# Optimization experiments

Hardware: AMD Instinct MI355X
Metric: run time of the kernel (lower is better)

## Reference

```python
import jax, jax.numpy as jnp
import numpy as np


def _branch(x2d, V, U, v2, v1, u2, u1):
    # x2d: [N, in]; V: [s, in]; U: [out, s]; scales are [1, dim]
    Vq = jnp.sign(V)
    Uq = jnp.sign(U)
    v1u2 = v1 * u2  # [1, s]
    h = (x2d * v2) @ Vq.T          # [N, s]
    y = (h * v1u2) @ Uq.T          # [N, out]
    return y * u1


def setup_inputs() -> dict:
    key = jax.random.key(0)
    ks = jax.random.split(key, 14)
    IN, OUT, S = 4096, 4096, 1024
    B, T = 4, 2048
    f = jax.random.normal
    return {
        "x":    f(ks[0], (B, T, IN), jnp.float32),
        "V":    f(ks[1], (S, IN), jnp.float32),
        "U":    f(ks[2], (OUT, S), jnp.float32),
        "v2":   f(ks[3], (1, IN), jnp.float32),
        "v1":   f(ks[4], (1, S), jnp.float32),
        "u2":   f(ks[5], (1, S), jnp.float32),
        "u1":   f(ks[6], (1, OUT), jnp.float32),
        "V_R":  f(ks[7], (S, IN), jnp.float32),
        "U_R":  f(ks[8], (OUT, S), jnp.float32),
        "v2_R": f(ks[9], (1, IN), jnp.float32),
        "v1_R": f(ks[10], (1, S), jnp.float32),
        "u2_R": f(ks[11], (1, S), jnp.float32),
        "u1_R": f(ks[12], (1, OUT), jnp.float32),
        "bias": f(ks[13], (OUT,), jnp.float32),
    }


def reference(x, V, U, v2, v1, u2, u1, V_R, U_R, v2_R, v1_R, u2_R, u1_R, bias):
    *lead, hidden = x.shape
    x2d = x.reshape(-1, hidden)
    y = _branch(x2d, V, U, v2, v1, u2, u1)
    y = y + _branch(x2d, V_R, U_R, v2_R, v1_R, u2_R, u1_R)
    y = y + bias
    return y.reshape(*lead, bias.shape[0])
```

## Files before the change

### kernel.cpp

```cpp
#include <hip/hip_runtime.h>
#include <hip/hip_bf16.h>
#include <stdint.h>

typedef __bf16 bf16_t;
typedef __attribute__((ext_vector_type(8))) __bf16 bf16x8;
typedef __attribute__((ext_vector_type(4))) float f32x4;

#define DIM_IN  4096
#define DIM_OUT 4096
#define DIM_S   1024
#define DIM_S2  2048
#define NROWS   8192

typedef const __attribute__((address_space(1))) void gvoid_t;
typedef __attribute__((address_space(3))) void lvoid_t;

__device__ __forceinline__ float signf(float v) {
    return (v > 0.f) ? 1.f : ((v < 0.f) ? -1.f : 0.f);
}


__global__ void cast_x_kernel(const float* __restrict__ x, bf16_t* __restrict__ xb) {
    int idx = blockIdx.x * blockDim.x + threadIdx.x;
    const float4* p = reinterpret_cast<const float4*>(x) + (size_t)idx * 2;
    float4 a = p[0], b = p[1];
    bf16x8 o;
    o[0] = (bf16_t)a.x; o[1] = (bf16_t)a.y; o[2] = (bf16_t)a.z; o[3] = (bf16_t)a.w;
    o[4] = (bf16_t)b.x; o[5] = (bf16_t)b.y; o[6] = (bf16_t)b.z; o[7] = (bf16_t)b.w;
    reinterpret_cast<bf16x8*>(xb)[idx] = o;
}

__global__ void build_vcat_kernel(const float* __restrict__ V, const float* __restrict__ v2,
                                  const float* __restrict__ V_R, const float* __restrict__ v2_R,
                                  bf16_t* __restrict__ out) {
    int idx = blockIdx.x * blockDim.x + threadIdx.x;
    int s2 = idx >> 9;
    int i0 = (idx & 511) * 8;
    const float* src; const float* sc;
    if (s2 < DIM_S) { src = V   + (size_t)s2 * DIM_IN;           sc = v2;   }
    else            { src = V_R + (size_t)(s2 - DIM_S) * DIM_IN; sc = v2_R; }
    float4 a  = *reinterpret_cast<const float4*>(src + i0);
    float4 b  = *reinterpret_cast<const float4*>(src + i0 + 4);
    float4 sa = *reinterpret_cast<const float4*>(sc + i0);
    float4 sb = *reinterpret_cast<const float4*>(sc + i0 + 4);
    bf16x8 o;
    o[0] = (bf16_t)(signf(a.x) * sa.x); o[1] = (bf16_t)(signf(a.y) * sa.y);
    o[2] = (bf16_t)(signf(a.z) * sa.z); o[3] = (bf16_t)(signf(a.w) * sa.w);
    o[4] = (bf16_t)(signf(b.x) * sb.x); o[5] = (bf16_t)(signf(b.y) * sb.y);
    o[6] = (bf16_t)(signf(b.z) * sb.z); o[7] = (bf16_t)(signf(b.w) * sb.w);
    reinterpret_cast<bf16x8*>(out)[idx] = o;
}

__global__ void build_wcat_kernel(const float* __restrict__ U, const float* __restrict__ v1,
                                  const float* __restrict__ u2, const float* __restrict__ u1,
                                  const float* __restrict__ U_R, const float* __restrict__ v1_R,
                                  const float* __restrict__ u2_R, const float* __restrict__ u1_R,
                                  bf16_t* __restrict__ out) {
    int idx = blockIdx.x * blockDim.x + threadIdx.x;
    int j  = idx >> 8;
    int s0 = (idx & 255) * 8;
    const float* srcU; const float* sv1; const float* su2; float amp;
    if (s0 < DIM_S) { srcU = U   + (size_t)j * DIM_S + s0; sv1 = v1 + s0;   su2 = u2 + s0;   amp = u1[j];   }
    else { int s = s0 - DIM_S;
           srcU = U_R + (size_t)j * DIM_S + s;  sv1 = v1_R + s; su2 = u2_R + s; amp = u1_R[j]; }
    float4 a  = *reinterpret_cast<const float4*>(srcU);
    float4 b  = *reinterpret_cast<const float4*>(srcU + 4);
    float4 va = *reinterpret_cast<const float4*>(sv1);
    float4 vb = *reinterpret_cast<const float4*>(sv1 + 4);
    float4 ua = *reinterpret_cast<const float4*>(su2);
    float4 ub = *reinterpret_cast<const float4*>(su2 + 4);
    bf16x8 o;
    o[0] = (bf16_t)(amp * va.x * ua.x * signf(a.x));
    o[1] = (bf16_t)(amp * va.y * ua.y * signf(a.y));
    o[2] = (bf16_t)(amp * va.z * ua.z * signf(a.z));
    o[3] = (bf16_t)(amp * va.w * ua.w * signf(a.w));
    o[4] = (bf16_t)(amp * vb.x * ub.x * signf(b.x));
    o[5] = (bf16_t)(amp * vb.y * ub.y * signf(b.y));
    o[6] = (bf16_t)(amp * vb.z * ub.z * signf(b.z));
    o[7] = (bf16_t)(amp * vb.w * ub.w * signf(b.w));
    reinterpret_cast<bf16x8*>(out)[idx] = o;
}


#define VMCNT0() do { asm volatile("s_waitcnt vmcnt(0)" ::: "memory"); \
                      __builtin_amdgcn_sched_barrier(0); } while (0)

template<int N, int K, bool OUT_BF16>
__global__ __launch_bounds__(512, 2) void gemm256_kernel(
        const bf16_t* __restrict__ A, const bf16_t* __restrict__ B,
        bf16_t* __restrict__ Cb, float* __restrict__ Cf,
        const float* __restrict__ bias) {
    extern __shared__ char lds[];
    constexpr int NT = K / 64;
    static_assert(NT >= 2, "K too small");
    const int tid  = threadIdx.x;
    const int wave = tid >> 6;
    const int lane = tid & 63;
    const int wr = wave >> 2;
    const int wc = wave & 3;

    const int nwg  = gridDim.x;
    const int orig = blockIdx.x;
    const int swz  = (orig & 7) * (nwg >> 3) + (orig >> 3);
    constexpr int NTX = N / 256;
    const int n0 = (swz % NTX) * 256;
    const int m0 = (swz / NTX) * 256;

    char* ldsA = lds;
    char* ldsB = lds + 65536;

    const char* gA[2]; const char* gB[2];
#pragma unroll
    for (int j = 0; j < 2; ++j) {
        int off = j * 8192 + wave * 1024 + lane * 16;
        int lg  = off ^ (((off >> 7) & 7) << 4);
        int row = lg >> 7;
        int cb  = lg & 127;
        gA[j] = (const char*)A + (size_t)(m0 + row) * (K * 2) + cb;
        gB[j] = (const char*)B + (size_t)(n0 + row) * (K * 2) + cb;
    }

#define STAGE_A(t_, mh) do { \
    int _lo = (((t_) & 1) << 15) + ((mh) << 14) + (wave << 10); \
    size_t _ga = (size_t)(mh) * (128 * K * 2) + (size_t)(t_) * 128; \
    __builtin_amdgcn_global_load_lds((gvoid_t*)(gA[0] + _ga), (lvoid_t*)(ldsA + _lo), 16, 0, 0); \
    __builtin_amdgcn_global_load_lds((gvoid_t*)(gA[1] + _ga), (lvoid_t*)(ldsA + _lo + 8192), 16, 0, 0); \
} while (0)
#define STAGE_B(t_, nh) do { \
    int _lo = (((t_) & 1) << 15) + ((nh) << 14) + (wave << 10); \
    size_t _ga = (size_t)(nh) * (128 * K * 2) + (size_t)(t_) * 128; \
    __builtin_amdgcn_global_load_lds((gvoid_t*)(gB[0] + _ga), (lvoid_t*)(ldsB + _lo), 16, 0, 0); \
    __builtin_amdgcn_global_load_lds((gvoid_t*)(gB[1] + _ga), (lvoid_t*)(ldsB + _lo + 8192), 16, 0, 0); \
} while (0)

    const int swzmask = (lane & 7) << 4;
    int abase0, abase1, bbase0, bbase1;
    {
        int araw = (lane & 15) * 128 + ((lane >> 4) << 4);
        abase0 = (araw ^ swzmask) + (wr << 14);
        abase1 = ((araw + 64) ^ swzmask) + (wr << 14);
        int braw = ((wc & 1) * 64 + (lane & 15)) * 128 + ((lane >> 4) << 4);
        bbase0 = (braw ^ swzmask) + ((wc >> 1) << 14);
        bbase1 = ((braw + 64) ^ swzmask) + ((wc >> 1) << 14);
    }

#define RD_A4(dst, base, mg, t_) do { \
    const int _sb = (((t_) & 1) << 15) + (base); \
    _Pragma("unroll") \
    for (int mi = 0; mi < 4; ++mi) \
        dst[mi] = *(const bf16x8*)(ldsA + _sb + ((mg) * 4 + mi) * 2048); \
} while (0)
#define RD_B4(dst, base, t_) do { \
    const int _sb = (((t_) & 1) << 15) + (base); \
    _Pragma("unroll") \
    for (int ni = 0; ni < 4; ++ni) \
        dst[ni] = *(const bf16x8*)(ldsB + _sb + ni * 2048); \
} while (0)
#define MFMA16(mg, AF, BF) do { \
    __builtin_amdgcn_s_setprio(1); \
    _Pragma("unroll") \
    for (int mi = 0; mi < 4; ++mi) \
        _Pragma("unroll") \
        for (int n = 0; n < 4; ++n) \
            acc[(mg) * 4 + mi][n] = __builtin_amdgcn_mfma_f32_16x16x32_bf16( \
                AF[mi], BF[n], acc[(mg) * 4 + mi][n], 0, 0, 0); \
    __builtin_amdgcn_s_setprio(0); \
} while (0)

    f32x4 acc[8][4];
#pragma unroll
    for (int m = 0; m < 8; ++m)
#pragma unroll
        for (int n = 0; n < 4; ++n)
            acc[m][n] = (f32x4){0.f, 0.f, 0.f, 0.f};

    bf16x8 afA[4], afB[4], bf0[4], bf1[4];

    STAGE_A(0, 0); STAGE_A(0, 1);
    STAGE_B(0, 0); STAGE_B(0, 1);
    VMCNT0();
    __builtin_amdgcn_s_barrier();

    for (int t = 0; t < NT; ++t) {
        const bool i1 = (t + 1 < NT);
        RD_A4(afA, abase0, 0, t);
        RD_B4(bf0, bbase0, t);
        if (i1) { STAGE_A(t + 1, 0); STAGE_A(t + 1, 1); }
        MFMA16(0, afA, bf0);
        RD_A4(afB, abase0, 1, t);
        if (i1) { STAGE_B(t + 1, 0); STAGE_B(t + 1, 1); }
        MFMA16(1, afB, bf0);
        RD_A4(afA, abase1, 0, t);
        RD_B4(bf1, bbase1, t);
        MFMA16(0, afA, bf1);
        RD_A4(afB, abase1, 1, t);
        MFMA16(1, afB, bf1);
        if (i1) { VMCNT0(); }
        __builtin_amdgcn_s_barrier();
    }

#undef RD_A4
#undef RD_B4
#undef MFMA16
#undef STAGE_A
#undef STAGE_B

    const int cr = (lane >> 4) << 2;
    const int cc = lane & 15;
#pragma unroll
    for (int m = 0; m < 8; ++m) {
        const int row = m0 + wr * 128 + m * 16 + cr;
#pragma unroll
        for (int n = 0; n < 4; ++n) {
            const int col = n0 + wc * 64 + n * 16 + cc;
            if (OUT_BF16) {
#pragma unroll
                for (int j = 0; j < 4; ++j)
                    Cb[(size_t)(row + j) * N + col] = (bf16_t)acc[m][n][j];
            } else {
                const float bv = bias[col];
#pragma unroll
                for (int j = 0; j < 4; ++j)
                    Cf[(size_t)(row + j) * N + col] = acc[m][n][j] + bv;
            }
        }
    }
}

extern "C" void kernel_launch(void* const* d_in, const int* in_sizes, int n_in,
                              void* d_out, int out_size, void* d_ws, size_t ws_size,
                              hipStream_t stream) {
    const float* x    = (const float*)d_in[0];
    const float* V    = (const float*)d_in[1];
    const float* U    = (const float*)d_in[2];
    const float* v2   = (const float*)d_in[3];
    const float* v1   = (const float*)d_in[4];
    const float* u2   = (const float*)d_in[5];
    const float* u1   = (const float*)d_in[6];
    const float* V_R  = (const float*)d_in[7];
    const float* U_R  = (const float*)d_in[8];
    const float* v2_R = (const float*)d_in[9];
    const float* v1_R = (const float*)d_in[10];
    const float* u2_R = (const float*)d_in[11];
    const float* u1_R = (const float*)d_in[12];
    const float* bias = (const float*)d_in[13];
    float* out = (float*)d_out;

    char* ws = (char*)d_ws;
    bf16_t* Xb   = (bf16_t*)(ws);
    bf16_t* Vcat = (bf16_t*)(ws + (size_t)64  * 1024 * 1024);
    bf16_t* Wcat = (bf16_t*)(ws + (size_t)80  * 1024 * 1024);
    bf16_t* Hb   = (bf16_t*)(ws + (size_t)96  * 1024 * 1024);

    (void)hipFuncSetAttribute((const void*)gemm256_kernel<DIM_S2, DIM_IN, true>,
                              hipFuncAttributeMaxDynamicSharedMemorySize, 131072);
    (void)hipFuncSetAttribute((const void*)gemm256_kernel<DIM_OUT, DIM_S2, false>,
                              hipFuncAttributeMaxDynamicSharedMemorySize, 131072);

    cast_x_kernel    <<<16384, 256, 0, stream>>>(x, Xb);
    build_vcat_kernel<<<4096, 256, 0, stream>>>(V, v2, V_R, v2_R, Vcat);
    build_wcat_kernel<<<4096, 256, 0, stream>>>(U, v1, u2, u1, U_R, v1_R, u2_R, u1_R, Wcat);

    gemm256_kernel<DIM_S2, DIM_IN, true>
        <<<(DIM_S2 / 256) * (NROWS / 256), 512, 131072, stream>>>(Xb, Vcat, Hb, nullptr, nullptr);
    gemm256_kernel<DIM_OUT, DIM_S2, false>
        <<<(DIM_OUT / 256) * (NROWS / 256), 512, 131072, stream>>>(Hb, Wcat, nullptr, out, bias);
}
```

Baseline: 289.8 us.

## Switch GEMM inner loop to 32x32x16 MFMA with software-pipelined LDS reads

Replaces the 16x16x32 bf16 MFMA tiles with 32x32x16 MFMA tiles, restructuring LDS fragment offsets, swizzle and accumulator layout to match. The K-loop is software-pipelined with double-buffered register fragments so LDS reads for the next k-slice overlap the current MFMAs, including prefetching across the barrier into the next stage. Larger MFMA tiles cut LDS read traffic per flop and instruction count. The risk is a wrong swizzle or layout mapping and a less coalesced epilogue store pattern.

```diff
diff --git a/kernel.cpp b/kernel.cpp
--- a/kernel.cpp
+++ b/kernel.cpp
@@ -5,6 +5,7 @@
 typedef __bf16 bf16_t;
 typedef __attribute__((ext_vector_type(8))) __bf16 bf16x8;
 typedef __attribute__((ext_vector_type(4))) float f32x4;
+typedef __attribute__((ext_vector_type(16))) float f32x16;
 
 #define DIM_IN  4096
 #define DIM_OUT 4096
@@ -133,95 +134,96 @@
     __builtin_amdgcn_global_load_lds((gvoid_t*)(gB[1] + _ga), (lvoid_t*)(ldsB + _lo + 8192), 16, 0, 0); \
 } while (0)
 
-    const int swzmask = (lane & 7) << 4;
-    int abase0, abase1, bbase0, bbase1;
-    {
-        int araw = (lane & 15) * 128 + ((lane >> 4) << 4);
-        abase0 = (araw ^ swzmask) + (wr << 14);
-        abase1 = ((araw + 64) ^ swzmask) + (wr << 14);
-        int braw = ((wc & 1) * 64 + (lane & 15)) * 128 + ((lane >> 4) << 4);
-        bbase0 = (braw ^ swzmask) + ((wc >> 1) << 14);
-        bbase1 = ((braw + 64) ^ swzmask) + ((wc >> 1) << 14);
-    }
-
-#define RD_A4(dst, base, mg, t_) do { \
-    const int _sb = (((t_) & 1) << 15) + (base); \
+    const int hi = lane >> 5;
+    const int lk = lane & 7;
+    int oA[4], oB[4];
+#pragma unroll
+    for (int kk = 0; kk < 4; ++kk) {
+        int slot = (((kk << 1) | hi) ^ lk) << 4;
+        oA[kk] = (wr << 14) + (lane & 31) * 128 + slot;
+        oB[kk] = 65536 + ((wc >> 1) << 14) + ((wc & 1) << 13) + (lane & 31) * 128 + slot;
+    }
+
+#define RD_A(dst, kk) do { \
     _Pragma("unroll") \
     for (int mi = 0; mi < 4; ++mi) \
-        dst[mi] = *(const bf16x8*)(ldsA + _sb + ((mg) * 4 + mi) * 2048); \
-} while (0)
-#define RD_B4(dst, base, t_) do { \
-    const int _sb = (((t_) & 1) << 15) + (base); \
-    _Pragma("unroll") \
-    for (int ni = 0; ni < 4; ++ni) \
-        dst[ni] = *(const bf16x8*)(ldsB + _sb + ni * 2048); \
-} while (0)
-#define MFMA16(mg, AF, BF) do { \
+        dst[mi] = *(const bf16x8*)(lds + oA[kk] + mi * 4096); \
+} while (0)
+#define RD_B(dst, kk) do { \
+    _Pragma("unroll") \
+    for (int ni = 0; ni < 2; ++ni) \
+        dst[ni] = *(const bf16x8*)(lds + oB[kk] + ni * 4096); \
+} while (0)
+#define FLIP() do { \
+    _Pragma("unroll") \
+    for (int kk = 0; kk < 4; ++kk) { oA[kk] ^= 0x8000; oB[kk] ^= 0x8000; } \
+} while (0)
+#define MFMA8(AF, BF) do { \
     __builtin_amdgcn_s_setprio(1); \
     _Pragma("unroll") \
     for (int mi = 0; mi < 4; ++mi) \
         _Pragma("unroll") \
-        for (int n = 0; n < 4; ++n) \
-            acc[(mg) * 4 + mi][n] = __builtin_amdgcn_mfma_f32_16x16x32_bf16( \
-                AF[mi], BF[n], acc[(mg) * 4 + mi][n], 0, 0, 0); \
+        for (int ni = 0; ni < 2; ++ni) \
+            acc[mi][ni] = __builtin_amdgcn_mfma_f32_32x32x16_bf16( \
+                AF[mi], BF[ni], acc[mi][ni], 0, 0, 0); \
     __builtin_amdgcn_s_setprio(0); \
 } while (0)
 
-    f32x4 acc[8][4];
-#pragma unroll
-    for (int m = 0; m < 8; ++m)
-#pragma unroll
-        for (int n = 0; n < 4; ++n)
-            acc[m][n] = (f32x4){0.f, 0.f, 0.f, 0.f};
-
-    bf16x8 afA[4], afB[4], bf0[4], bf1[4];
+    f32x16 acc[4][2];
+#pragma unroll
+    for (int m = 0; m < 4; ++m)
+#pragma unroll
+        for (int n = 0; n < 2; ++n)
+#pragma unroll
+            for (int j = 0; j < 16; ++j)
+                acc[m][n][j] = 0.f;
+
+    bf16x8 afP[4], afQ[4], bfP[2], bfQ[2];
 
     STAGE_A(0, 0); STAGE_A(0, 1);
     STAGE_B(0, 0); STAGE_B(0, 1);
     VMCNT0();
     __builtin_amdgcn_s_barrier();
+    RD_A(afP, 0); RD_B(bfP, 0);
 
     for (int t = 0; t < NT; ++t) {
         const bool i1 = (t + 1 < NT);
-        RD_A4(afA, abase0, 0, t);
-        RD_B4(bf0, bbase0, t);
         if (i1) { STAGE_A(t + 1, 0); STAGE_A(t + 1, 1); }
-        MFMA16(0, afA, bf0);
-        RD_A4(afB, abase0, 1, t);
+        RD_A(afQ, 1); RD_B(bfQ, 1);
+        MFMA8(afP, bfP);
         if (i1) { STAGE_B(t + 1, 0); STAGE_B(t + 1, 1); }
-        MFMA16(1, afB, bf0);
-        RD_A4(afA, abase1, 0, t);
-        RD_B4(bf1, bbase1, t);
-        MFMA16(0, afA, bf1);
-        RD_A4(afB, abase1, 1, t);
-        MFMA16(1, afB, bf1);
+        RD_A(afP, 2); RD_B(bfP, 2);
+        MFMA8(afQ, bfQ);
+        RD_A(afQ, 3); RD_B(bfQ, 3);
+        MFMA8(afP, bfP);
         if (i1) { VMCNT0(); }
         __builtin_amdgcn_s_barrier();
-    }
-
-#undef RD_A4
-#undef RD_B4
-#undef MFMA16
+        if (i1) { FLIP(); RD_A(afP, 0); RD_B(bfP, 0); }
+        MFMA8(afQ, bfQ);
+    }
+
+#undef RD_A
+#undef RD_B
+#undef FLIP
+#undef MFMA8
 #undef STAGE_A
 #undef STAGE_B
 
-    const int cr = (lane >> 4) << 2;
-    const int cc = lane & 15;
-#pragma unroll
-    for (int m = 0; m < 8; ++m) {
-        const int row = m0 + wr * 128 + m * 16 + cr;
-#pragma unroll
-        for (int n = 0; n < 4; ++n) {
-            const int col = n0 + wc * 64 + n * 16 + cc;
-            if (OUT_BF16) {
-#pragma unroll
-                for (int j = 0; j < 4; ++j)
-                    Cb[(size_t)(row + j) * N + col] = (bf16_t)acc[m][n][j];
-            } else {
-                const float bv = bias[col];
-#pragma unroll
-                for (int j = 0; j < 4; ++j)
-                    Cf[(size_t)(row + j) * N + col] = acc[m][n][j] + bv;
+    const int cc = lane & 31;
+    const int rhi = (lane >> 5) * 4;
+#pragma unroll
+    for (int m = 0; m < 4; ++m) {
+#pragma unroll
+        for (int n = 0; n < 2; ++n) {
+            const int col = n0 + wc * 64 + n * 32 + cc;
+            const float bv = OUT_BF16 ? 0.f : bias[col];
+#pragma unroll
+            for (int j = 0; j < 16; ++j) {
+                const int row = m0 + wr * 128 + m * 32 + (j & 3) + 8 * (j >> 2) + rhi;
+                if (OUT_BF16)
+                    Cb[(size_t)row * N + col] = (bf16_t)acc[m][n][j];
+                else
+                    Cf[(size_t)row * N + col] = acc[m][n][j] + bv;
             }
         }
     }
```

New measurement: 307.3 us. 6.0% more time.

## Phase GEMM main loop with workgroup barriers and explicit LDS waits

Applied to the files above, without the earlier changes.

Restructures the K-loop of the 256-tile GEMM into four phases. Each phase issues LDS fragment reads, then a workgroup barrier and an lgkmcnt(0) wait, then the MFMA block. A single A/B fragment register set is reused instead of double register buffers, which cuts register pressure. The aim is to synchronise waves so MFMA and memory phases interleave across waves, and the cost is many extra barriers and lost overlap of LDS reads with MFMA inside each wave. VMCNT0 now runs unconditionally, including on the last iteration.

```diff
diff --git a/kernel.cpp b/kernel.cpp
--- a/kernel.cpp
+++ b/kernel.cpp
@@ -84,6 +84,8 @@
 
 #define VMCNT0() do { asm volatile("s_waitcnt vmcnt(0)" ::: "memory"); \
                       __builtin_amdgcn_sched_barrier(0); } while (0)
+#define LGKM0()  do { asm volatile("s_waitcnt lgkmcnt(0)" ::: "memory"); \
+                      __builtin_amdgcn_sched_barrier(0); } while (0)
 
 template<int N, int K, bool OUT_BF16>
 __global__ __launch_bounds__(512, 2) void gemm256_kernel(
@@ -174,7 +176,7 @@
         for (int n = 0; n < 4; ++n)
             acc[m][n] = (f32x4){0.f, 0.f, 0.f, 0.f};
 
-    bf16x8 afA[4], afB[4], bf0[4], bf1[4];
+    bf16x8 af[4], bf[4];
 
     STAGE_A(0, 0); STAGE_A(0, 1);
     STAGE_B(0, 0); STAGE_B(0, 1);
@@ -183,19 +185,30 @@
 
     for (int t = 0; t < NT; ++t) {
         const bool i1 = (t + 1 < NT);
-        RD_A4(afA, abase0, 0, t);
-        RD_B4(bf0, bbase0, t);
+        RD_A4(af, abase0, 0, t);
+        RD_B4(bf, bbase0, t);
         if (i1) { STAGE_A(t + 1, 0); STAGE_A(t + 1, 1); }
-        MFMA16(0, afA, bf0);
-        RD_A4(afB, abase0, 1, t);
+        __builtin_amdgcn_s_barrier();
+        LGKM0();
+        MFMA16(0, af, bf);
+        __builtin_amdgcn_s_barrier();
+        RD_A4(af, abase0, 1, t);
         if (i1) { STAGE_B(t + 1, 0); STAGE_B(t + 1, 1); }
-        MFMA16(1, afB, bf0);
-        RD_A4(afA, abase1, 0, t);
-        RD_B4(bf1, bbase1, t);
-        MFMA16(0, afA, bf1);
-        RD_A4(afB, abase1, 1, t);
-        MFMA16(1, afB, bf1);
-        if (i1) { VMCNT0(); }
+        __builtin_amdgcn_s_barrier();
+        LGKM0();
+        MFMA16(1, af, bf);
+        __builtin_amdgcn_s_barrier();
+        RD_A4(af, abase1, 0, t);
+        RD_B4(bf, bbase1, t);
+        __builtin_amdgcn_s_barrier();
+        LGKM0();
+        MFMA16(0, af, bf);
+        __builtin_amdgcn_s_barrier();
+        RD_A4(af, abase1, 1, t);
+        __builtin_amdgcn_s_barrier();
+        LGKM0();
+        MFMA16(1, af, bf);
+        VMCNT0();
         __builtin_amdgcn_s_barrier();
     }
 
```

Measured after the change: 307.5 us. 1.06x slower.

## Shrink GEMM tiles to 128x128 with 4 waves and software-pipelined LDS reads

Applied to the files above, without the earlier changes.

Replaces the 256x256 tile, 8-wave GEMM with a 128x128 tile, 4-wave version using 64KB of LDS. The inner loop now prefetches the next k-step's LDS fragments across the barrier, giving a register double-buffered schedule, and drops the setprio hints. Smaller tiles quadruple the workgroup count and may improve occupancy and tail balance. In exchange, each tile reuses global data less, so global and L2 traffic per FLOP roughly doubles.

```diff
diff --git a/kernel.cpp b/kernel.cpp
--- a/kernel.cpp
+++ b/kernel.cpp
@@ -84,9 +84,10 @@
 
 #define VMCNT0() do { asm volatile("s_waitcnt vmcnt(0)" ::: "memory"); \
                       __builtin_amdgcn_sched_barrier(0); } while (0)
+#define SB0()    __builtin_amdgcn_sched_barrier(0)
 
 template<int N, int K, bool OUT_BF16>
-__global__ __launch_bounds__(512, 2) void gemm256_kernel(
+__global__ __launch_bounds__(256, 2) void gemm128_kernel(
         const bf16_t* __restrict__ A, const bf16_t* __restrict__ B,
         bf16_t* __restrict__ Cb, float* __restrict__ Cf,
         const float* __restrict__ bias) {
@@ -96,23 +97,23 @@
     const int tid  = threadIdx.x;
     const int wave = tid >> 6;
     const int lane = tid & 63;
-    const int wr = wave >> 2;
-    const int wc = wave & 3;
+    const int wr = wave >> 1;
+    const int wc = wave & 1;
 
     const int nwg  = gridDim.x;
     const int orig = blockIdx.x;
     const int swz  = (orig & 7) * (nwg >> 3) + (orig >> 3);
-    constexpr int NTX = N / 256;
-    const int n0 = (swz % NTX) * 256;
-    const int m0 = (swz / NTX) * 256;
+    constexpr int NTX = N / 128;
+    const int n0 = (swz % NTX) * 128;
+    const int m0 = (swz / NTX) * 128;
 
     char* ldsA = lds;
-    char* ldsB = lds + 65536;
-
-    const char* gA[2]; const char* gB[2];
-#pragma unroll
-    for (int j = 0; j < 2; ++j) {
-        int off = j * 8192 + wave * 1024 + lane * 16;
+    char* ldsB = lds + 32768;
+
+    const char* gA[4]; const char* gB[4];
+#pragma unroll
+    for (int j = 0; j < 4; ++j) {
+        int off = j * 4096 + wave * 1024 + lane * 16;
         int lg  = off ^ (((off >> 7) & 7) << 4);
         int row = lg >> 7;
         int cb  = lg & 127;
@@ -120,83 +121,79 @@
         gB[j] = (const char*)B + (size_t)(n0 + row) * (K * 2) + cb;
     }
 
-#define STAGE_A(t_, mh) do { \
-    int _lo = (((t_) & 1) << 15) + ((mh) << 14) + (wave << 10); \
-    size_t _ga = (size_t)(mh) * (128 * K * 2) + (size_t)(t_) * 128; \
-    __builtin_amdgcn_global_load_lds((gvoid_t*)(gA[0] + _ga), (lvoid_t*)(ldsA + _lo), 16, 0, 0); \
-    __builtin_amdgcn_global_load_lds((gvoid_t*)(gA[1] + _ga), (lvoid_t*)(ldsA + _lo + 8192), 16, 0, 0); \
-} while (0)
-#define STAGE_B(t_, nh) do { \
-    int _lo = (((t_) & 1) << 15) + ((nh) << 14) + (wave << 10); \
-    size_t _ga = (size_t)(nh) * (128 * K * 2) + (size_t)(t_) * 128; \
-    __builtin_amdgcn_global_load_lds((gvoid_t*)(gB[0] + _ga), (lvoid_t*)(ldsB + _lo), 16, 0, 0); \
-    __builtin_amdgcn_global_load_lds((gvoid_t*)(gB[1] + _ga), (lvoid_t*)(ldsB + _lo + 8192), 16, 0, 0); \
+#define STAGE_A(t_) do { \
+    int _lo = (((t_) & 1) << 14) + (wave << 10); \
+    _Pragma("unroll") \
+    for (int _j = 0; _j < 4; ++_j) \
+        __builtin_amdgcn_global_load_lds((gvoid_t*)(gA[_j] + (size_t)(t_) * 128), \
+                                         (lvoid_t*)(ldsA + _lo + _j * 4096), 16, 0, 0); \
+} while (0)
+#define STAGE_B(t_) do { \
+    int _lo = (((t_) & 1) << 14) + (wave << 10); \
+    _Pragma("unroll") \
+    for (int _j = 0; _j < 4; ++_j) \
+        __builtin_amdgcn_global_load_lds((gvoid_t*)(gB[_j] + (size_t)(t_) * 128), \
+                                         (lvoid_t*)(ldsB + _lo + _j * 4096), 16, 0, 0); \
 } while (0)
 
     const int swzmask = (lane & 7) << 4;
     int abase0, abase1, bbase0, bbase1;
     {
-        int araw = (lane & 15) * 128 + ((lane >> 4) << 4);
-        abase0 = (araw ^ swzmask) + (wr << 14);
-        abase1 = ((araw + 64) ^ swzmask) + (wr << 14);
-        int braw = ((wc & 1) * 64 + (lane & 15)) * 128 + ((lane >> 4) << 4);
-        bbase0 = (braw ^ swzmask) + ((wc >> 1) << 14);
-        bbase1 = ((braw + 64) ^ swzmask) + ((wc >> 1) << 14);
-    }
-
-#define RD_A4(dst, base, mg, t_) do { \
-    const int _sb = (((t_) & 1) << 15) + (base); \
+        int araw = (wr * 64 + (lane & 15)) * 128 + ((lane >> 4) << 4);
+        abase0 = (araw ^ swzmask);
+        abase1 = ((araw + 64) ^ swzmask);
+        int braw = (wc * 64 + (lane & 15)) * 128 + ((lane >> 4) << 4);
+        bbase0 = (braw ^ swzmask);
+        bbase1 = ((braw + 64) ^ swzmask);
+    }
+
+#define RD_A4(dst, base, t_) do { \
+    const int _sb = (((t_) & 1) << 14) + (base); \
     _Pragma("unroll") \
     for (int mi = 0; mi < 4; ++mi) \
-        dst[mi] = *(const bf16x8*)(ldsA + _sb + ((mg) * 4 + mi) * 2048); \
+        dst[mi] = *(const bf16x8*)(ldsA + _sb + mi * 2048); \
 } while (0)
 #define RD_B4(dst, base, t_) do { \
-    const int _sb = (((t_) & 1) << 15) + (base); \
+    const int _sb = (((t_) & 1) << 14) + (base); \
     _Pragma("unroll") \
     for (int ni = 0; ni < 4; ++ni) \
         dst[ni] = *(const bf16x8*)(ldsB + _sb + ni * 2048); \
 } while (0)
-#define MFMA16(mg, AF, BF) do { \
-    __builtin_amdgcn_s_setprio(1); \
+#define MFMA16(AF, BF) do { \
     _Pragma("unroll") \
     for (int mi = 0; mi < 4; ++mi) \
         _Pragma("unroll") \
         for (int n = 0; n < 4; ++n) \
-            acc[(mg) * 4 + mi][n] = __builtin_amdgcn_mfma_f32_16x16x32_bf16( \
-                AF[mi], BF[n], acc[(mg) * 4 + mi][n], 0, 0, 0); \
-    __builtin_amdgcn_s_setprio(0); \
-} while (0)
-
-    f32x4 acc[8][4];
-#pragma unroll
-    for (int m = 0; m < 8; ++m)
+            acc[mi][n] = __builtin_amdgcn_mfma_f32_16x16x32_bf16( \
+                AF[mi], BF[n], acc[mi][n], 0, 0, 0); \
+} while (0)
+
+    f32x4 acc[4][4];
+#pragma unroll
+    for (int m = 0; m < 4; ++m)
 #pragma unroll
         for (int n = 0; n < 4; ++n)
             acc[m][n] = (f32x4){0.f, 0.f, 0.f, 0.f};
 
-    bf16x8 afA[4], afB[4], bf0[4], bf1[4];
-
-    STAGE_A(0, 0); STAGE_A(0, 1);
-    STAGE_B(0, 0); STAGE_B(0, 1);
+    bf16x8 afP[4], afQ[4], bfP[4], bfQ[4];
+
+    STAGE_A(0); STAGE_B(0);
     VMCNT0();
     __builtin_amdgcn_s_barrier();
+    RD_A4(afP, abase0, 0); RD_B4(bfP, bbase0, 0);
 
     for (int t = 0; t < NT; ++t) {
         const bool i1 = (t + 1 < NT);
-        RD_A4(afA, abase0, 0, t);
-        RD_B4(bf0, bbase0, t);
-        if (i1) { STAGE_A(t + 1, 0); STAGE_A(t + 1, 1); }
-        MFMA16(0, afA, bf0);
-        RD_A4(afB, abase0, 1, t);
-        if (i1) { STAGE_B(t + 1, 0); STAGE_B(t + 1, 1); }
-        MFMA16(1, afB, bf0);
-        RD_A4(afA, abase1, 0, t);
-        RD_B4(bf1, bbase1, t);
-        MFMA16(0, afA, bf1);
-        RD_A4(afB, abase1, 1, t);
-        MFMA16(1, afB, bf1);
+        if (i1) { STAGE_A(t + 1); STAGE_B(t + 1); }
+        RD_A4(afQ, abase1, t);
+        RD_B4(bfQ, bbase1, t);
+        SB0();
+        MFMA16(afP, bfP);
         if (i1) { VMCNT0(); }
         __builtin_amdgcn_s_barrier();
+        if (i1) { RD_A4(afP, abase0, t + 1); RD_B4(bfP, bbase0, t + 1); }
+        SB0();
+        MFMA16(afQ, bfQ);
     }
 
 #undef RD_A4
@@ -208,8 +205,8 @@
     const int cr = (lane >> 4) << 2;
     const int cc = lane & 15;
 #pragma unroll
-    for (int m = 0; m < 8; ++m) {
-        const int row = m0 + wr * 128 + m * 16 + cr;
+    for (int m = 0; m < 4; ++m) {
+        const int row = m0 + wr * 64 + m * 16 + cr;
 #pragma unroll
         for (int n = 0; n < 4; ++n) {
             const int col = n0 + wc * 64 + n * 16 + cc;
@@ -252,17 +249,17 @@
     bf16_t* Wcat = (bf16_t*)(ws + (size_t)80  * 1024 * 1024);
     bf16_t* Hb   = (bf16_t*)(ws + (size_t)96  * 1024 * 1024);
 
-    (void)hipFuncSetAttribute((const void*)gemm256_kernel<DIM_S2, DIM_IN, true>,
-                              hipFuncAttributeMaxDynamicSharedMemorySize, 131072);
-    (void)hipFuncSetAttribute((const void*)gemm256_kernel<DIM_OUT, DIM_S2, false>,
-                              hipFuncAttributeMaxDynamicSharedMemorySize, 131072);
+    (void)hipFuncSetAttribute((const void*)gemm128_kernel<DIM_S2, DIM_IN, true>,
+                              hipFuncAttributeMaxDynamicSharedMemorySize, 65536);
+    (void)hipFuncSetAttribute((const void*)gemm128_kernel<DIM_OUT, DIM_S2, false>,
+                              hipFuncAttributeMaxDynamicSharedMemorySize, 65536);
 
     cast_x_kernel    <<<16384, 256, 0, stream>>>(x, Xb);
     build_vcat_kernel<<<4096, 256, 0, stream>>>(V, v2, V_R, v2_R, Vcat);
     build_wcat_kernel<<<4096, 256, 0, stream>>>(U, v1, u2, u1, U_R, v1_R, u2_R, u1_R, Wcat);
 
-    gemm256_kernel<DIM_S2, DIM_IN, true>
-        <<<(DIM_S2 / 256) * (NROWS / 256), 512, 131072, stream>>>(Xb, Vcat, Hb, nullptr, nullptr);
-    gemm256_kernel<DIM_OUT, DIM_S2, false>
-        <<<(DIM_OUT / 256) * (NROWS / 256), 512, 131072, stream>>>(Hb, Wcat, nullptr, out, bias);
-}
+    gemm128_kernel<DIM_S2, DIM_IN, true>
+        <<<(DIM_S2 / 128) * (NROWS / 128), 256, 65536, stream>>>(Xb, Vcat, Hb, nullptr, nullptr);
+    gemm128_kernel<DIM_OUT, DIM_S2, false>
+        <<<(DIM_OUT / 128) * (NROWS / 128), 256, 65536, stream>>>(Hb, Wcat, nullptr, out, bias);
+}
```

After: 351.1 us. +21.2%, slower.
